# Performance work log

Measured on AMD Instinct MI355X. Metric: run time of the kernel, lower is better.

The kernel has to match this reference:

```python
import jax, jax.numpy as jnp
import numpy as np

B, S, H = 1, 4096, 2048
HQ, HKV, D = 8, 4, 256
WIN = 1024          # sliding window
SOFTCAP = 50.0      # attn logit softcapping
EPS = 1e-6          # rms_norm_eps
ROPE_THETA = 10000.0


def setup_inputs() -> dict:
    key = jax.random.key(0)
    ks = jax.random.split(key, 6)
    hidden_states = jax.random.normal(ks[0], (B, S, H), dtype=jnp.float32)
    # RoPE cos/sin tables, shape [B, S, D]
    inv_freq = 1.0 / (ROPE_THETA ** (jnp.arange(0, D, 2, dtype=jnp.float32) / D))
    pos = jnp.arange(S, dtype=jnp.float32)
    freqs = pos[:, None] * inv_freq[None, :]          # [S, D/2]
    emb = jnp.concatenate([freqs, freqs], axis=-1)    # [S, D]
    cos = jnp.broadcast_to(jnp.cos(emb)[None], (B, S, D)).astype(jnp.float32)
    sin = jnp.broadcast_to(jnp.sin(emb)[None], (B, S, D)).astype(jnp.float32)
    qpos = jnp.arange(S)[:, None]
    kpos = jnp.arange(S)[None, :]
    diff = qpos - kpos
    allowed = (diff >= 0) & (diff < WIN)
    attention_mask = jnp.where(allowed, 0.0, -1e9).astype(jnp.float32)[None, None]
    attention_mask = jnp.broadcast_to(attention_mask, (B, 1, S, S))
    w_scale = 0.02
    Wq = jax.random.normal(ks[1], (HQ * D, H), dtype=jnp.float32) * w_scale
    Wk = jax.random.normal(ks[2], (HKV * D, H), dtype=jnp.float32) * w_scale
    Wv = jax.random.normal(ks[3], (HKV * D, H), dtype=jnp.float32) * w_scale
    Wo = jax.random.normal(ks[4], (H, HQ * D), dtype=jnp.float32) * w_scale
    q_norm_w = jnp.ones((D,), dtype=jnp.float32)
    k_norm_w = jnp.ones((D,), dtype=jnp.float32)
    return {"hidden_states": hidden_states, "cos": cos, "sin": sin,
            "attention_mask": attention_mask, "Wq": Wq, "Wk": Wk, "Wv": Wv,
            "Wo": Wo, "q_norm_w": q_norm_w, "k_norm_w": k_norm_w}


def _rms_norm(x, weight=None):
    # Gemma4 RMSNorm in fp32: x * rsqrt(mean(x^2) + eps) [* weight]
    ms = jnp.mean(x * x, axis=-1, keepdims=True) + EPS
    y = x * jax.lax.rsqrt(ms)
    return y * weight if weight is not None else y


def _rope(x, cos, sin):
    # x: [B,S,Hn,D]; cos/sin: [B,S,D] -> unsqueeze at dim 2
    x1, x2 = jnp.split(x, 2, axis=-1)
    rot = jnp.concatenate([-x2, x1], axis=-1)
    return x * cos[:, :, None, :] + rot * sin[:, :, None, :]


def reference(hidden_states, cos, sin, attention_mask, Wq, Wk, Wv, Wo, q_norm_w, k_norm_w):
    n_rep = HQ // HKV
    q = (hidden_states @ Wq.T).reshape(B, S, HQ, D)     # [B,S,HQ,D]
    q = _rms_norm(q, q_norm_w)
    q = _rope(q, cos, sin).transpose(0, 2, 1, 3)        # [B,HQ,S,D]
    k = (hidden_states @ Wk.T).reshape(B, S, HKV, D)
    k = _rms_norm(k, k_norm_w)
    k = _rope(k, cos, sin).transpose(0, 2, 1, 3)        # [B,HKV,S,D]
    v = (hidden_states @ Wv.T).reshape(B, S, HKV, D)
    v = _rms_norm(v).transpose(0, 2, 1, 3)              # [B,HKV,S,D]
    # repeat_kv (GQA)
    k = jnp.repeat(k, n_rep, axis=1)                    # [B,HQ,S,D]
    v = jnp.repeat(v, n_rep, axis=1)
    scores = jnp.einsum('bhqd,bhkd->bhqk', q, k)        # scaling = 1.0
    scores = jnp.tanh(scores / SOFTCAP) * SOFTCAP       # softcap
    scores = scores + attention_mask
    attn = jax.nn.softmax(scores.astype(jnp.float32), axis=-1).astype(q.dtype)
    out = jnp.einsum('bhqk,bhkd->bhqd', attn, v)        # [B,HQ,S,D]
    out = out.transpose(0, 2, 1, 3).reshape(B, S, HQ * D)
    return out @ Wo.T                                   # [B,S,H]
```

## Files before the change

kernel.cpp:

```cpp
#include <hip/hip_runtime.h>

#define S_LEN 4096
#define HID   2048
#define NHQ   8
#define NKV   4
#define DHEAD 256
#define WIN   1024

typedef __attribute__((ext_vector_type(4))) float     floatx4;
typedef __attribute__((ext_vector_type(8))) _Float16  halfx8;

__device__ __forceinline__ unsigned short f2h(float f){
  union { _Float16 h; unsigned short u; } cv; cv.h = (_Float16)f; return cv.u;
}
__device__ __forceinline__ float h2f(unsigned short u){
  union { unsigned short u; _Float16 h; } cv; cv.u = u; return (float)cv.h;
}

__device__ __forceinline__ void gld_lds16(const void* g, void* l){
  __builtin_amdgcn_global_load_lds((const __attribute__((address_space(1))) void*)g,
                                   (__attribute__((address_space(3))) void*)l, 16, 0, 0);
}

__global__ __launch_bounds__(256) void cvt_all(const float* __restrict__ hs,
                                               const float* __restrict__ Wq,
                                               const float* __restrict__ Wk,
                                               const float* __restrict__ Wv,
                                               const float* __restrict__ Wo,
                                               unsigned short* __restrict__ h_h,
                                               unsigned short* __restrict__ w_qkv,
                                               unsigned short* __restrict__ wo){
  int bid = blockIdx.x;
  const float* src;
  unsigned short* dst;
  size_t i;
  if (bid < 8192){
    i = ((size_t)bid * 256 + threadIdx.x) * 4;
    src = hs + i; dst = h_h + i;
  } else if (bid < 16384){
    i = ((size_t)(bid - 8192) * 256 + threadIdx.x) * 4;
    int row = (int)(i >> 11), col = (int)(i & 2047);
    src = ((row < 2048) ? (Wq + ((size_t)row << 11))
         : (row < 3072) ? (Wk + ((size_t)(row - 2048) << 11))
                        : (Wv + ((size_t)(row - 3072) << 11))) + col;
    dst = w_qkv + i;
  } else {
    i = ((size_t)(bid - 16384) * 256 + threadIdx.x) * 4;
    src = Wo + i; dst = wo + i;
  }
  float4 v = *(const float4*)src;
  *(ushort4*)dst = make_ushort4(f2h(v.x), f2h(v.y), f2h(v.z), f2h(v.w));
}

template<int OUT_F32>
__global__ __launch_bounds__(256, 2) void gemm_ht(const unsigned short* __restrict__ A,
                                                  const unsigned short* __restrict__ B,
                                                  void* __restrict__ Cv,
                                                  int ldC, int K){
  __shared__ __align__(16) unsigned short As[128 * 32];
  __shared__ __align__(16) unsigned short Bs[128 * 32];
  const int t = threadIdx.x, w = t >> 6, lane = t & 63;
  const int quad = lane >> 4, l15 = lane & 15;
  const int l2 = lane >> 2, g8 = (lane & 3) * 8;
  const int wm = w >> 1, wn = w & 1;
  const int bm0 = blockIdx.y * 128, bn0 = blockIdx.x * 128;

  const floatx4 zf = {0.f, 0.f, 0.f, 0.f};
  floatx4 acc[4][4];
#pragma unroll
  for (int mi = 0; mi < 4; ++mi)
#pragma unroll
    for (int ni = 0; ni < 4; ++ni) acc[mi][ni] = zf;

  for (int k0 = 0; k0 < K; k0 += 32){
#pragma unroll
    for (int j = 0; j < 2; ++j){
      int ch  = j * 4 + w;
      int row = ch * 16 + l2;
      gld_lds16(A + (size_t)(bm0 + row) * K + k0 + g8, &As[ch * 512]);
      gld_lds16(B + (size_t)(bn0 + row) * K + k0 + g8, &Bs[ch * 512]);
    }
    __syncthreads();
    halfx8 af[4], bf[4];
#pragma unroll
    for (int mi = 0; mi < 4; ++mi) af[mi] = *(const halfx8*)&As[(wm*64 + mi*16 + l15)*32 + quad*8];
#pragma unroll
    for (int ni = 0; ni < 4; ++ni) bf[ni] = *(const halfx8*)&Bs[(wn*64 + ni*16 + l15)*32 + quad*8];
#pragma unroll
    for (int mi = 0; mi < 4; ++mi)
#pragma unroll
      for (int ni = 0; ni < 4; ++ni)
        acc[mi][ni] = __builtin_amdgcn_mfma_f32_16x16x32_f16(af[mi], bf[ni], acc[mi][ni], 0, 0, 0);
    __syncthreads();
  }
#pragma unroll
  for (int mi = 0; mi < 4; ++mi)
#pragma unroll
    for (int ni = 0; ni < 4; ++ni)
#pragma unroll
      for (int r = 0; r < 4; ++r){
        int m = bm0 + wm*64 + mi*16 + quad*4 + r;
        int n = bn0 + wn*64 + ni*16 + l15;
        float v = acc[mi][ni][r];
        if (OUT_F32) ((float*)Cv)[(size_t)m * ldC + n] = v;
        else         ((unsigned short*)Cv)[(size_t)m * ldC + n] = f2h(v);
      }
}

__global__ __launch_bounds__(256) void qkv_post(const unsigned short* __restrict__ qkvh,
                                                const float* __restrict__ cosb,
                                                const float* __restrict__ sinb,
                                                const float* __restrict__ qnw,
                                                const float* __restrict__ knw,
                                                unsigned short* __restrict__ Qf,
                                                unsigned short* __restrict__ Kf,
                                                unsigned short* __restrict__ Vf){
  int gw   = blockIdx.x * 4 + (threadIdx.x >> 6);
  int lane = threadIdx.x & 63;
  int hh = gw & 15, s = gw >> 4;
  int colbase = (hh < 8) ? hh * 256 : (hh < 12 ? 2048 + (hh - 8) * 256 : 3072 + (hh - 12) * 256);

  ushort4 raw = *(const ushort4*)(qkvh + (size_t)s * 4096 + colbase + lane * 4);
  float x0 = h2f(raw.x), x1 = h2f(raw.y), x2 = h2f(raw.z), x3 = h2f(raw.w);
  float ss = x0*x0 + x1*x1 + x2*x2 + x3*x3;
#pragma unroll
  for (int off = 32; off; off >>= 1) ss += __shfl_xor(ss, off);
  float inv = rsqrtf(ss * (1.0f / 256.0f) + 1e-6f);

  if (hh < 12){
    const float* wp = (hh < 8) ? qnw : knw;
    float4 wv = *(const float4*)(wp + lane * 4);
    float y[4] = { x0*inv*wv.x, x1*inv*wv.y, x2*inv*wv.z, x3*inv*wv.w };
    float4 cv = *(const float4*)(cosb + (size_t)s * 256 + lane * 4);
    float4 sv = *(const float4*)(sinb + (size_t)s * 256 + lane * 4);
    float cj[4] = {cv.x, cv.y, cv.z, cv.w};
    float sj[4] = {sv.x, sv.y, sv.z, sv.w};
    unsigned short oh[4];
#pragma unroll
    for (int j = 0; j < 4; ++j){
      float oth = __shfl_xor(y[j], 32);
      float rot = (lane < 32) ? -oth : oth;
      oh[j] = f2h(y[j] * cj[j] + rot * sj[j]);
    }
    ushort4 r = make_ushort4(oh[0], oh[1], oh[2], oh[3]);
    if (hh < 8) *(ushort4*)(Qf + (size_t)(hh       * S_LEN + s) * DHEAD + lane * 4) = r;
    else        *(ushort4*)(Kf + (size_t)((hh - 8) * S_LEN + s) * DHEAD + lane * 4) = r;
  } else {
    ushort4 r = make_ushort4(f2h(x0*inv), f2h(x1*inv), f2h(x2*inv), f2h(x3*inv));
    *(ushort4*)(Vf + (size_t)((hh - 12) * S_LEN + s) * DHEAD + lane * 4) = r;
  }
}

__global__ __launch_bounds__(256) void transpose_v(const unsigned short* __restrict__ v,
                                                   unsigned short* __restrict__ vt){
  __shared__ unsigned short tile[64][68];
  int kv = blockIdx.z, d0 = blockIdx.x * 64, s0 = blockIdx.y * 64;
  int t = threadIdx.x;
  int r = t >> 4, c4 = (t & 15) * 4;
#pragma unroll
  for (int i = 0; i < 4; ++i){
    int row = r + i * 16;
    ushort4 xx = *(const ushort4*)(v + (size_t)(kv * S_LEN + s0 + row) * DHEAD + d0 + c4);
    tile[row][c4] = xx.x; tile[row][c4+1] = xx.y; tile[row][c4+2] = xx.z; tile[row][c4+3] = xx.w;
  }
  __syncthreads();
#pragma unroll
  for (int i = 0; i < 4; ++i){
    int dr = r + i * 16;
    ushort4 yy = make_ushort4(tile[c4][dr], tile[c4+1][dr], tile[c4+2][dr], tile[c4+3][dr]);
    *(ushort4*)(vt + (size_t)(kv * DHEAD + d0 + dr) * S_LEN + s0 + c4) = yy;
  }
}

__global__ __launch_bounds__(256, 3) void attn_win(const unsigned short* __restrict__ Qg,
                                                   const unsigned short* __restrict__ Kg,
                                                   const unsigned short* __restrict__ Vt,
                                                   unsigned short* __restrict__ Og){
  __shared__ __align__(16) unsigned short Ks[8 * 32 * 32];
  __shared__ __align__(16) unsigned short Vts[256 * 32];
  __shared__ __align__(16) unsigned short Pb[4][16 * 48];

  const int h = blockIdx.y, kv = h >> 1;
  const int q0 = blockIdx.x * 64;
  const int t = threadIdx.x, w = t >> 6, lane = t & 63;
  const int quad = lane >> 4, l15 = lane & 15;
  const int l2 = lane >> 2, g8 = (lane & 3) * 8;
  const int qw0 = q0 + w * 16;

  halfx8 qf[8];
#pragma unroll
  for (int c = 0; c < 8; ++c)
    qf[c] = *(const halfx8*)(Qg + (size_t)(h * S_LEN + qw0 + l15) * DHEAD + c*32 + quad*8);

  const floatx4 zf = {0.f, 0.f, 0.f, 0.f};
  floatx4 oacc[16];
#pragma unroll
  for (int dt = 0; dt < 16; ++dt) oacc[dt] = zf;
  float m_run[4], l_run[4];
#pragma unroll
  for (int r = 0; r < 4; ++r){ m_run[r] = -50.0f; l_run[r] = 0.0f; }

  int kt_lo = q0 / 32 - 32; if (kt_lo < 0) kt_lo = 0;
  int kt_hi = q0 / 32 + 1;

  for (int kt = kt_lo; kt <= kt_hi; ++kt){
    const int key0 = kt * 32;
#pragma unroll
    for (int j = 0; j < 4; ++j){
      int ch = j * 4 + w;
      int krow = (ch & 1) * 16 + l2;
      int cb = ch >> 1;
      gld_lds16(Kg + (size_t)(kv * S_LEN + key0 + krow) * DHEAD + cb * 32 + g8, &Ks[ch * 512]);
      int drow = ch * 16 + l2;
      gld_lds16(Vt + (size_t)(kv * DHEAD + drow) * S_LEN + key0 + g8, &Vts[ch * 512]);
    }
    __syncthreads();

    if (key0 <= qw0 + 15 && key0 + 31 >= qw0 - (WIN - 1)){
      floatx4 sc[2];
      sc[0] = zf; sc[1] = zf;
#pragma unroll
      for (int c = 0; c < 8; ++c){
#pragma unroll
        for (int nt = 0; nt < 2; ++nt){
          halfx8 kf = *(const halfx8*)&Ks[c * 1024 + (nt*16 + l15) * 32 + quad * 8];
          sc[nt] = __builtin_amdgcn_mfma_f32_16x16x32_f16(qf[c], kf, sc[nt], 0, 0, 0);
        }
      }
      const bool tfull = (key0 + 31 <= qw0) && (qw0 + 15 - key0 < WIN);
      float x[2][4];
#pragma unroll
      for (int nt = 0; nt < 2; ++nt)
#pragma unroll
        for (int r = 0; r < 4; ++r){
          float v = sc[nt][r];
          float e = __expf(v * 0.04f);
          v = 50.0f - 100.0f / (e + 1.0f);
          if (!tfull){
            int qi = qw0 + quad*4 + r;
            int ki = key0 + nt*16 + l15;
            bool ok = (ki <= qi) && (qi - ki < WIN);
            v = ok ? v : -__builtin_inff();
          }
          x[nt][r] = v;
        }
      float alpha[4];
#pragma unroll
      for (int r = 0; r < 4; ++r){
        float tm = fmaxf(x[0][r], x[1][r]);
        tm = fmaxf(tm, __shfl_xor(tm, 1));
        tm = fmaxf(tm, __shfl_xor(tm, 2));
        tm = fmaxf(tm, __shfl_xor(tm, 4));
        tm = fmaxf(tm, __shfl_xor(tm, 8));
        float mo = m_run[r];
        float mn = fmaxf(mo, tm);
        float a = __expf(mo - mn);
        m_run[r] = mn; alpha[r] = a;
        float p0 = __expf(x[0][r] - mn);
        float p1 = __expf(x[1][r] - mn);
        x[0][r] = p0; x[1][r] = p1;
        float ls = p0 + p1;
        ls += __shfl_xor(ls, 1);
        ls += __shfl_xor(ls, 2);
        ls += __shfl_xor(ls, 4);
        ls += __shfl_xor(ls, 8);
        l_run[r] = l_run[r] * a + ls;
      }
#pragma unroll
      for (int nt = 0; nt < 2; ++nt)
#pragma unroll
        for (int r = 0; r < 4; ++r)
          Pb[w][(quad*4 + r) * 48 + nt*16 + l15] = f2h(x[nt][r]);
#pragma unroll
      for (int dt = 0; dt < 16; ++dt){
        floatx4 v = oacc[dt];
        v.x *= alpha[0]; v.y *= alpha[1]; v.z *= alpha[2]; v.w *= alpha[3];
        oacc[dt] = v;
      }
      halfx8 pf = *(const halfx8*)&Pb[w][l15 * 48 + quad * 8];
#pragma unroll
      for (int dt = 0; dt < 16; ++dt){
        halfx8 vf = *(const halfx8*)&Vts[(dt*16 + l15) * 32 + quad * 8];
        oacc[dt] = __builtin_amdgcn_mfma_f32_16x16x32_f16(pf, vf, oacc[dt], 0, 0, 0);
      }
    }
    __syncthreads();
  }
#pragma unroll
  for (int r = 0; r < 4; ++r){
    float rl = 1.0f / l_run[r];
    int srow = qw0 + quad*4 + r;
#pragma unroll
    for (int dt = 0; dt < 16; ++dt)
      Og[(size_t)srow * (NHQ * DHEAD) + h * DHEAD + dt*16 + l15] = f2h(oacc[dt][r] * rl);
  }
}

extern "C" void kernel_launch(void* const* d_in, const int* in_sizes, int n_in,
                              void* d_out, int out_size, void* d_ws, size_t ws_size,
                              hipStream_t stream){
  const float* hs   = (const float*)d_in[0];
  const float* cosb = (const float*)d_in[1];
  const float* sinb = (const float*)d_in[2];
  const float* Wq   = (const float*)d_in[4];
  const float* Wk   = (const float*)d_in[5];
  const float* Wv   = (const float*)d_in[6];
  const float* Wo   = (const float*)d_in[7];
  const float* qnw  = (const float*)d_in[8];
  const float* knw  = (const float*)d_in[9];
  float* out = (float*)d_out;

  const size_t MB = 1024ull * 1024ull;
  char* ws = (char*)d_ws;
  unsigned short* h_h   = (unsigned short*)(ws);
  unsigned short* w_qkv = (unsigned short*)(ws + 16 * MB);
  unsigned short* wo    = (unsigned short*)(ws + 32 * MB);
  unsigned short* qkvh  = (unsigned short*)(ws + 40 * MB);
  unsigned short* Qf    = (unsigned short*)(ws);
  unsigned short* Kf    = (unsigned short*)(ws + 16 * MB);
  unsigned short* Vf    = (unsigned short*)(ws + 24 * MB);
  unsigned short* vt    = (unsigned short*)(ws + 40 * MB);
  unsigned short* ob    = (unsigned short*)(ws + 48 * MB);

  cvt_all<<<20480, 256, 0, stream>>>(hs, Wq, Wk, Wv, Wo, h_h, w_qkv, wo);

  gemm_ht<0><<<dim3(32, 32), 256, 0, stream>>>(h_h, w_qkv, qkvh, 4096, 2048);

  qkv_post<<<16384, 256, 0, stream>>>(qkvh, cosb, sinb, qnw, knw, Qf, Kf, Vf);
  transpose_v<<<dim3(4, 64, 4), 256, 0, stream>>>(Vf, vt);

  attn_win<<<dim3(64, 8), 256, 0, stream>>>(Qf, Kf, vt, ob);

  gemm_ht<1><<<dim3(16, 32), 256, 0, stream>>>(ob, wo, out, 2048, 2048);
}
```

Before: 444.2 us.

## Double-buffer K/V tiles in attention and skip rescale when max is unchanged

The windowed attention kernel now keeps two LDS buffers for K and V^T and issues the async global-to-LDS loads for the next key tile before computing on the current one. This overlaps memory latency with MFMA work and drops one barrier per iteration. It also rescales the output accumulators only when some row's running max has grown, checked wave-wide. Row sums are kept per lane and reduced across lanes once at the end rather than every tile. The doubled LDS footprint forces the occupancy hint down from 3 to 2 blocks per CU.

```diff
diff --git a/kernel.cpp b/kernel.cpp
--- a/kernel.cpp
+++ b/kernel.cpp
@@ -172,12 +172,12 @@
   }
 }
 
-__global__ __launch_bounds__(256, 3) void attn_win(const unsigned short* __restrict__ Qg,
+__global__ __launch_bounds__(256, 2) void attn_win(const unsigned short* __restrict__ Qg,
                                                    const unsigned short* __restrict__ Kg,
                                                    const unsigned short* __restrict__ Vt,
                                                    unsigned short* __restrict__ Og){
-  __shared__ __align__(16) unsigned short Ks[8 * 32 * 32];
-  __shared__ __align__(16) unsigned short Vts[256 * 32];
+  __shared__ __align__(16) unsigned short Ks[2][8 * 32 * 32];
+  __shared__ __align__(16) unsigned short Vts[2][256 * 32];
   __shared__ __align__(16) unsigned short Pb[4][16 * 48];
 
   const int h = blockIdx.y, kv = h >> 1;
@@ -196,26 +196,40 @@
   floatx4 oacc[16];
 #pragma unroll
   for (int dt = 0; dt < 16; ++dt) oacc[dt] = zf;
-  float m_run[4], l_run[4];
-#pragma unroll
-  for (int r = 0; r < 4; ++r){ m_run[r] = -50.0f; l_run[r] = 0.0f; }
+  float m_run[4], l_part[4];
+#pragma unroll
+  for (int r = 0; r < 4; ++r){ m_run[r] = -50.0f; l_part[r] = 0.0f; }
 
   int kt_lo = q0 / 32 - 32; if (kt_lo < 0) kt_lo = 0;
   int kt_hi = q0 / 32 + 1;
 
+  const size_t kbase = (size_t)kv * S_LEN * DHEAD;
+  const size_t vbase = (size_t)kv * DHEAD * S_LEN;
+
+#define STAGE(KT, B)                                                              \
+  {                                                                               \
+    const int key0_ = (KT) * 32;                                                  \
+    _Pragma("unroll")                                                             \
+    for (int j = 0; j < 4; ++j){                                                  \
+      int ch = j * 4 + w;                                                         \
+      int krow = (ch & 1) * 16 + l2;                                              \
+      int cb = ch >> 1;                                                           \
+      gld_lds16(Kg + kbase + (size_t)(key0_ + krow) * DHEAD + cb * 32 + g8,       \
+                &Ks[B][ch * 512]);                                                \
+      int drow = ch * 16 + l2;                                                    \
+      gld_lds16(Vt + vbase + (size_t)drow * S_LEN + key0_ + g8,                   \
+                &Vts[B][ch * 512]);                                               \
+    }                                                                             \
+  }
+
+  STAGE(kt_lo, 0);
+
   for (int kt = kt_lo; kt <= kt_hi; ++kt){
+    const int cur = (kt - kt_lo) & 1;
+    __syncthreads();
+    if (kt < kt_hi) STAGE(kt + 1, cur ^ 1);
+
     const int key0 = kt * 32;
-#pragma unroll
-    for (int j = 0; j < 4; ++j){
-      int ch = j * 4 + w;
-      int krow = (ch & 1) * 16 + l2;
-      int cb = ch >> 1;
-      gld_lds16(Kg + (size_t)(kv * S_LEN + key0 + krow) * DHEAD + cb * 32 + g8, &Ks[ch * 512]);
-      int drow = ch * 16 + l2;
-      gld_lds16(Vt + (size_t)(kv * DHEAD + drow) * S_LEN + key0 + g8, &Vts[ch * 512]);
-    }
-    __syncthreads();
-
     if (key0 <= qw0 + 15 && key0 + 31 >= qw0 - (WIN - 1)){
       floatx4 sc[2];
       sc[0] = zf; sc[1] = zf;
@@ -223,7 +237,7 @@
       for (int c = 0; c < 8; ++c){
 #pragma unroll
         for (int nt = 0; nt < 2; ++nt){
-          halfx8 kf = *(const halfx8*)&Ks[c * 1024 + (nt*16 + l15) * 32 + quad * 8];
+          halfx8 kf = *(const halfx8*)&Ks[cur][c * 1024 + (nt*16 + l15) * 32 + quad * 8];
           sc[nt] = __builtin_amdgcn_mfma_f32_16x16x32_f16(qf[c], kf, sc[nt], 0, 0, 0);
         }
       }
@@ -239,56 +253,63 @@
           if (!tfull){
             int qi = qw0 + quad*4 + r;
             int ki = key0 + nt*16 + l15;
-            bool ok = (ki <= qi) && (qi - ki < WIN);
-            v = ok ? v : -__builtin_inff();
+            v = ((ki <= qi) && (qi - ki < WIN)) ? v : -__builtin_inff();
           }
           x[nt][r] = v;
         }
-      float alpha[4];
+      float tm[4]; bool grew = false;
 #pragma unroll
       for (int r = 0; r < 4; ++r){
-        float tm = fmaxf(x[0][r], x[1][r]);
-        tm = fmaxf(tm, __shfl_xor(tm, 1));
-        tm = fmaxf(tm, __shfl_xor(tm, 2));
-        tm = fmaxf(tm, __shfl_xor(tm, 4));
-        tm = fmaxf(tm, __shfl_xor(tm, 8));
-        float mo = m_run[r];
-        float mn = fmaxf(mo, tm);
-        float a = __expf(mo - mn);
-        m_run[r] = mn; alpha[r] = a;
-        float p0 = __expf(x[0][r] - mn);
-        float p1 = __expf(x[1][r] - mn);
-        x[0][r] = p0; x[1][r] = p1;
-        float ls = p0 + p1;
-        ls += __shfl_xor(ls, 1);
-        ls += __shfl_xor(ls, 2);
-        ls += __shfl_xor(ls, 4);
-        ls += __shfl_xor(ls, 8);
-        l_run[r] = l_run[r] * a + ls;
+        float m2 = fmaxf(x[0][r], x[1][r]);
+        m2 = fmaxf(m2, __shfl_xor(m2, 1));
+        m2 = fmaxf(m2, __shfl_xor(m2, 2));
+        m2 = fmaxf(m2, __shfl_xor(m2, 4));
+        m2 = fmaxf(m2, __shfl_xor(m2, 8));
+        tm[r] = m2;
+        grew = grew || (m2 > m_run[r]);
+      }
+      if (__any(grew)){
+        float al[4];
+#pragma unroll
+        for (int r = 0; r < 4; ++r){
+          float mn = fmaxf(m_run[r], tm[r]);
+          al[r] = __expf(m_run[r] - mn);
+          m_run[r] = mn;
+          l_part[r] *= al[r];
+        }
+#pragma unroll
+        for (int dt = 0; dt < 16; ++dt){
+          floatx4 v = oacc[dt];
+          v.x *= al[0]; v.y *= al[1]; v.z *= al[2]; v.w *= al[3];
+          oacc[dt] = v;
+        }
       }
 #pragma unroll
       for (int nt = 0; nt < 2; ++nt)
 #pragma unroll
-        for (int r = 0; r < 4; ++r)
-          Pb[w][(quad*4 + r) * 48 + nt*16 + l15] = f2h(x[nt][r]);
+        for (int r = 0; r < 4; ++r){
+          float p = __expf(x[nt][r] - m_run[r]);
+          l_part[r] += p;
+          Pb[w][(quad*4 + r) * 48 + nt*16 + l15] = f2h(p);
+        }
+      halfx8 pf = *(const halfx8*)&Pb[w][l15 * 48 + quad * 8];
 #pragma unroll
       for (int dt = 0; dt < 16; ++dt){
-        floatx4 v = oacc[dt];
-        v.x *= alpha[0]; v.y *= alpha[1]; v.z *= alpha[2]; v.w *= alpha[3];
-        oacc[dt] = v;
-      }
-      halfx8 pf = *(const halfx8*)&Pb[w][l15 * 48 + quad * 8];
-#pragma unroll
-      for (int dt = 0; dt < 16; ++dt){
-        halfx8 vf = *(const halfx8*)&Vts[(dt*16 + l15) * 32 + quad * 8];
+        halfx8 vf = *(const halfx8*)&Vts[cur][(dt*16 + l15) * 32 + quad * 8];
         oacc[dt] = __builtin_amdgcn_mfma_f32_16x16x32_f16(pf, vf, oacc[dt], 0, 0, 0);
       }
     }
-    __syncthreads();
-  }
+  }
+#undef STAGE
+
 #pragma unroll
   for (int r = 0; r < 4; ++r){
-    float rl = 1.0f / l_run[r];
+    float l = l_part[r];
+    l += __shfl_xor(l, 1);
+    l += __shfl_xor(l, 2);
+    l += __shfl_xor(l, 4);
+    l += __shfl_xor(l, 8);
+    float rl = 1.0f / l;
     int srow = qw0 + quad*4 + r;
 #pragma unroll
     for (int dt = 0; dt < 16; ++dt)
```

Measured after the change: 431.1 us. 2.9% less time.
